# Kernel optimization log

Measured on AMD Instinct MI355X. Metric: run time of the kernel, lower is better.

Reference implementation:

```python
import jax, jax.numpy as jnp
import numpy as np

GATE_THRESH = 0.4
ALPHA_FN = lambda L: 1.0 - 1.0 / L  # length-adaptive alpha, called with actual L
EPS_NORM = 1e-12  # F.normalize eps
EPS_LN = 1e-5     # LayerNorm eps


def setup_inputs() -> dict:
    key = jax.random.key(0)
    B, L, H, V = 64, 2048, 128, 32000
    ks = jax.random.split(key, 8)
    s = lambda k, shape, fan: jax.random.normal(k, shape, jnp.float32) * (1.0 / np.sqrt(fan))
    return {
        "seq": jax.random.randint(ks[0], (B, L), 0, V, dtype=jnp.int64),
        "embed_w": jax.random.normal(ks[1], (V, H), jnp.float32) * 0.02,
        "ff_w1": s(ks[2], (2 * H, H), H), "ff_b1": jnp.zeros((2 * H,), jnp.float32),
        "ff_w2": s(ks[3], (H, 2 * H), 2 * H), "ff_b2": jnp.zeros((H,), jnp.float32),
        "ln_g": jnp.ones((H,), jnp.float32), "ln_b": jnp.zeros((H,), jnp.float32),
        "kp_w": s(ks[4], (H, H), H),
        "rp_w": s(ks[5], (H, H), H), "rp_b": jnp.zeros((H,), jnp.float32),
        "out_w": s(ks[6], (V, H), H), "out_b": jnpp if False else jnp.zeros((V,), jnp.float32),
    }


def reference(seq, embed_w, ff_w1, ff_b1, ff_w2, ff_b2, ln_g, ln_b, kp_w, rp_w, rp_b, out_w, out_b):
    h = embed_w[seq]                                            # [B,L,H]
    ff = jnp.maximum(h @ ff_w1.T + ff_b1, 0.0) @ ff_w2.T + ff_b2
    x = h + ff
    mu = x.mean(-1, keepdims=True)
    var = x.var(-1, keepdims=True)                              # biased, as LayerNorm
    h = (x - mu) / jnp.sqrt(var + EPS_LN) * ln_g + ln_b
    B, L, H = h.shape
    alpha = ALPHA_FN(L)
    k_all = jnp.einsum('blh,oh->blo', h, kp_w)                  # kp has no bias

    def step(M, k):                                             # M:[B,H,H], k:[B,H]
        kn = k / jnp.maximum(jnp.linalg.norm(k, axis=-1, keepdims=True), EPS_NORM)
        vp = jnp.einsum('bij,bj->bi', M, kn)
        d = k - vp
        delta = d[:, :, None] * kn[:, None, :]                  # outer product [B,H,H]
        fire = (jnp.linalg.norm(d, axis=-1) >= GATE_THRESH * jnp.linalg.norm(k, axis=-1)).astype(k.dtype)
        return M + (1.0 - alpha) * fire[:, None, None] * delta, None

    M0 = jnp.zeros((B, H, H), h.dtype)
    M, _ = jax.lax.scan(step, M0, jnp.swapaxes(k_all[:, :-1, :], 0, 1))  # scan over L-1 steps
    q = k_all[:, -1, :]
    read = jnp.einsum('bij,bj->bi', M, q)
    return (read @ rp_w.T + rp_b) @ out_w.T + out_b             # [B,V]
```

## Files before the change

### kernel.cpp

```cpp
#include <hip/hip_runtime.h>
#include <hip/hip_bf16.h>
#include <stdint.h>

#define Bn 64
#define Ln 2048
#define Hn 128
#define Vn 32000
#define THn 256
#define LAMBDA_ (1.0f/2048.0f)
#define CC 32
#define NCH (Ln/CC)
#define KP  132
#define KTS 36
#define VS  132
#define VPW (CC*VS)
#define ADS 131
#define ADW (CC*ADS+4)
#define GS  36
#define GXS 33
#define MSR 36
#define MSW 576
#define HS  132

typedef short bf16x8 __attribute__((ext_vector_type(8)));
typedef float f32x4  __attribute__((ext_vector_type(4)));

__device__ __forceinline__ float rdlane(float v, int s) {
  return __int_as_float(__builtin_amdgcn_readlane(__float_as_int(v), s));
}

template <int CTRL>
__device__ __forceinline__ float dpp_add(float x) {
  int t = __builtin_amdgcn_update_dpp(0, __float_as_int(x), CTRL, 0xf, 0xf, false);
  return x + __int_as_float(t);
}
__device__ __forceinline__ float wave_sum64(float x) {
  x = dpp_add<0x111>(x);
  x = dpp_add<0x112>(x);
  x = dpp_add<0x114>(x);
  x = dpp_add<0x118>(x);
  x = dpp_add<0x142>(x);
  x = dpp_add<0x143>(x);
  return rdlane(x, 63);
}

__device__ __forceinline__ uint32_t packhl(float x) {
  uint32_t bx = __float_as_uint(x);
  float hf = __uint_as_float(bx & 0xFFFF0000u);
  uint32_t bl = __float_as_uint(x - hf);
  return (bx >> 16) | (bl & 0xFFFF0000u);
}
__device__ __forceinline__ float unpackhl(uint32_t u) {
  return __uint_as_float(u << 16) + __uint_as_float(u & 0xFFFF0000u);
}

struct FragHL { bf16x8 h; bf16x8 l; };
__device__ __forceinline__ FragHL mkfrag(const uint32_t* u) {
  union { uint32_t a[4]; bf16x8 v; } H, L;
  H.a[0] = __builtin_amdgcn_perm(u[1], u[0], 0x05040100u);
  H.a[1] = __builtin_amdgcn_perm(u[3], u[2], 0x05040100u);
  H.a[2] = __builtin_amdgcn_perm(u[5], u[4], 0x05040100u);
  H.a[3] = __builtin_amdgcn_perm(u[7], u[6], 0x05040100u);
  L.a[0] = __builtin_amdgcn_perm(u[1], u[0], 0x07060302u);
  L.a[1] = __builtin_amdgcn_perm(u[3], u[2], 0x07060302u);
  L.a[2] = __builtin_amdgcn_perm(u[5], u[4], 0x07060302u);
  L.a[3] = __builtin_amdgcn_perm(u[7], u[6], 0x07060302u);
  FragHL f; f.h = H.v; f.l = L.v; return f;
}

__device__ __forceinline__ void ld8(const uint32_t* p, uint32_t* u) {
  const uint4 a = *reinterpret_cast<const uint4*>(p);
  const uint4 b = *reinterpret_cast<const uint4*>(p + 4);
  u[0]=a.x; u[1]=a.y; u[2]=a.z; u[3]=a.w;
  u[4]=b.x; u[5]=b.y; u[6]=b.z; u[7]=b.w;
}

__device__ __forceinline__ bf16x8 asbf(uint4 u) {
  union { uint4 a; bf16x8 v; } c; c.a = u; return c.v;
}

__device__ __forceinline__ f32x4 mfma16(bf16x8 a, bf16x8 b, f32x4 c) {
  return __builtin_amdgcn_mfma_f32_16x16x32_bf16(a, b, c, 0, 0, 0);
}

__device__ __forceinline__ void gload_lds4(const uint32_t* g, uint32_t* l) {
  __builtin_amdgcn_global_load_lds(
      (const __attribute__((address_space(1))) void*)g,
      (__attribute__((address_space(3))) void*)l, 4, 0, 0);
}

__global__ __launch_bounds__(256) void p0_pack(
    const float* __restrict__ w1, const float* __restrict__ w2,
    const float* __restrict__ kp, uint32_t* __restrict__ wp)
{
  const int id = blockIdx.x*256 + threadIdx.x;
  const float* src; uint32_t *dh, *dl; int p;
  if (id < 16384)      { src = w1; p = id;         dh = wp;         dl = wp+16384; }
  else if (id < 32768) { src = w2; p = id-16384;   dh = wp+32768;   dl = wp+49152; }
  else                 { src = kp; p = id-32768;   dh = wp+65536;   dl = wp+73728; }
  const float x0 = src[2*p], x1 = src[2*p+1];
  const uint32_t b0 = __float_as_uint(x0), b1 = __float_as_uint(x1);
  const float l0f = x0 - __uint_as_float(b0 & 0xFFFF0000u);
  const float l1f = x1 - __uint_as_float(b1 & 0xFFFF0000u);
  dh[p] = (b0 >> 16) | ((b1 >> 16) << 16);
  dl[p] = (__float_as_uint(l0f) >> 16) | ((__float_as_uint(l1f) >> 16) << 16);
}

__global__ __launch_bounds__(256, 2) void p1_fused(
    const int* __restrict__ seq,
    const float* __restrict__ embed_w,
    const uint32_t* __restrict__ wp,
    const float* __restrict__ ff_b1, const float* __restrict__ ff_b2,
    const float* __restrict__ ln_g, const float* __restrict__ ln_b,
    uint32_t* __restrict__ knp_all, float* __restrict__ norm_all)
{
  __shared__ __align__(16) uint32_t h_p[64*HS];
  __shared__ __align__(16) uint32_t u_p[64*HS];
  __shared__ float part1[256], part2[256];
  __shared__ float mul[64], rsl[64];
  __shared__ int sid[64];

  const int tid  = threadIdx.x;
  const int lane = tid & 63;
  const int w    = __builtin_amdgcn_readfirstlane(tid >> 6);
  const int q4   = lane >> 4;
  const int m16  = lane & 15;
  const int tile0 = blockIdx.x * 64;

  const uint32_t* w1h = wp;
  const uint32_t* w1l = wp + 16384;
  const uint32_t* w2h = wp + 32768;
  const uint32_t* w2l = wp + 49152;
  const uint32_t* kph = wp + 65536;
  const uint32_t* kpl = wp + 73728;

  if (tid < 64) sid[tid] = seq[tile0 + tid];
  __syncthreads();

  {
    const int t = tid >> 2, part = tid & 3;
    const float4* erow =
        reinterpret_cast<const float4*>(embed_w + (size_t)sid[t]*Hn) + part*8;
    #pragma unroll
    for (int c = 0; c < 8; ++c) {
      float4 v = erow[c];
      int j = part*32 + c*4;
      h_p[t*HS+j+0] = packhl(v.x); h_p[t*HS+j+1] = packhl(v.y);
      h_p[t*HS+j+2] = packhl(v.z); h_p[t*HS+j+3] = packhl(v.w);
    }
  }
  __syncthreads();

  f32x4 acc2[4][2];
  #pragma unroll
  for (int tt=0;tt<4;++tt)
    #pragma unroll
    for (int ct=0;ct<2;++ct) acc2[tt][ct] = (f32x4){0.f,0.f,0.f,0.f};

  #pragma unroll 1
  for (int ho=0; ho<2; ++ho) {
    #pragma unroll 1
    for (int tt=0; tt<4; ++tt) {
      FragHL fa[4];
      #pragma unroll
      for (int kk=0;kk<4;++kk) {
        uint32_t ua[8];
        ld8(&h_p[(16*tt+m16)*HS + 32*kk + 8*q4], ua);
        fa[kk] = mkfrag(ua);
      }
      #pragma unroll
      for (int ct=0; ct<2; ++ct) {
        const int ob = 128*ho + 32*w + 16*ct;
        f32x4 a = (f32x4){0.f,0.f,0.f,0.f};
        #pragma unroll
        for (int kk=0;kk<4;++kk) {
          const size_t wi = (size_t)(ob+m16)*64 + 16*kk + 4*q4;
          bf16x8 bh = asbf(*reinterpret_cast<const uint4*>(&w1h[wi]));
          bf16x8 bl = asbf(*reinterpret_cast<const uint4*>(&w1l[wi]));
          a = mfma16(fa[kk].h, bh, a);
          a = mfma16(fa[kk].h, bl, a);
          a = mfma16(fa[kk].l, bh, a);
        }
        const float bb = ff_b1[ob + m16];
        #pragma unroll
        for (int reg=0;reg<4;++reg) {
          float uv = fmaxf(a[reg] + bb, 0.f);
          u_p[(16*tt+4*q4+reg)*HS + 32*w + 16*ct + m16] = packhl(uv);
        }
      }
    }
    __syncthreads();
    #pragma unroll 1
    for (int tt=0; tt<4; ++tt) {
      FragHL fu[4];
      #pragma unroll
      for (int kk=0;kk<4;++kk) {
        uint32_t ua[8];
        ld8(&u_p[(16*tt+m16)*HS + 32*kk + 8*q4], ua);
        fu[kk] = mkfrag(ua);
      }
      #pragma unroll
      for (int ct=0; ct<2; ++ct) {
        const int ib = 32*w + 16*ct;
        f32x4 a = acc2[tt][ct];
        #pragma unroll
        for (int kk=0;kk<4;++kk) {
          const size_t wi = (size_t)(ib+m16)*128 + 64*ho + 16*kk + 4*q4;
          bf16x8 bh = asbf(*reinterpret_cast<const uint4*>(&w2h[wi]));
          bf16x8 bl = asbf(*reinterpret_cast<const uint4*>(&w2l[wi]));
          a = mfma16(fu[kk].h, bh, a);
          a = mfma16(fu[kk].h, bl, a);
          a = mfma16(fu[kk].l, bh, a);
        }
        acc2[tt][ct] = a;
      }
    }
    __syncthreads();
  }

  float xx[4][2][4];
  #pragma unroll
  for (int tt=0;tt<4;++tt)
    #pragma unroll
    for (int ct=0;ct<2;++ct) {
      const int col = 32*w + 16*ct + m16;
      const float b2 = ff_b2[col];
      #pragma unroll
      for (int reg=0;reg<4;++reg) {
        const float hval = unpackhl(h_p[(16*tt+4*q4+reg)*HS + col]);
        xx[tt][ct][reg] = acc2[tt][ct][reg] + b2 + hval;
      }
    }
  #pragma unroll
  for (int tt=0;tt<4;++tt)
    #pragma unroll
    for (int reg=0;reg<4;++reg) {
      float s1 = xx[tt][0][reg] + xx[tt][1][reg];
      float s2 = xx[tt][0][reg]*xx[tt][0][reg] + xx[tt][1][reg]*xx[tt][1][reg];
      s1 += __shfl_xor(s1,1); s1 += __shfl_xor(s1,2);
      s1 += __shfl_xor(s1,4); s1 += __shfl_xor(s1,8);
      s2 += __shfl_xor(s2,1); s2 += __shfl_xor(s2,2);
      s2 += __shfl_xor(s2,4); s2 += __shfl_xor(s2,8);
      if (m16==0) {
        part1[w*64 + 16*tt+4*q4+reg] = s1;
        part2[w*64 + 16*tt+4*q4+reg] = s2;
      }
    }
  __syncthreads();
  if (tid < 64) {
    const float mu = (part1[tid]+part1[64+tid]+part1[128+tid]+part1[192+tid])*(1.0f/128.0f);
    const float ms = (part2[tid]+part2[64+tid]+part2[128+tid]+part2[192+tid])*(1.0f/128.0f);
    mul[tid] = mu;
    rsl[tid] = rsqrtf(ms - mu*mu + 1e-5f);
  }
  __syncthreads();

  #pragma unroll
  for (int tt=0;tt<4;++tt)
    #pragma unroll
    for (int ct=0;ct<2;++ct) {
      const int col = 32*w + 16*ct + m16;
      const float g = ln_g[col], bb = ln_b[col];
      #pragma unroll
      for (int reg=0;reg<4;++reg) {
        const int tok = 16*tt+4*q4+reg;
        const float hn = (xx[tt][ct][reg] - mul[tok])*rsl[tok]*g + bb;
        h_p[tok*HS + col] = packhl(hn);
      }
    }
  __syncthreads();

  f32x4 ak[4][2];
  #pragma unroll 1
  for (int tt=0;tt<4;++tt) {
    FragHL fh[4];
    #pragma unroll
    for (int kk=0;kk<4;++kk) {
      uint32_t ua[8];
      ld8(&h_p[(16*tt+m16)*HS + 32*kk + 8*q4], ua);
      fh[kk] = mkfrag(ua);
    }
    #pragma unroll
    for (int ct=0;ct<2;++ct) {
      const int ob = 32*w + 16*ct;
      f32x4 a = (f32x4){0.f,0.f,0.f,0.f};
      #pragma unroll
      for (int kk=0;kk<4;++kk) {
        const size_t wi = (size_t)(ob+m16)*64 + 16*kk + 4*q4;
        bf16x8 bh = asbf(*reinterpret_cast<const uint4*>(&kph[wi]));
        bf16x8 bl = asbf(*reinterpret_cast<const uint4*>(&kpl[wi]));
        a = mfma16(fh[kk].h, bh, a);
        a = mfma16(fh[kk].h, bl, a);
        a = mfma16(fh[kk].l, bh, a);
      }
      ak[tt][ct] = a;
    }
  }
  #pragma unroll
  for (int tt=0;tt<4;++tt)
    #pragma unroll
    for (int reg=0;reg<4;++reg) {
      float s = ak[tt][0][reg]*ak[tt][0][reg] + ak[tt][1][reg]*ak[tt][1][reg];
      s += __shfl_xor(s,1); s += __shfl_xor(s,2);
      s += __shfl_xor(s,4); s += __shfl_xor(s,8);
      if (m16==0) part1[w*64 + 16*tt+4*q4+reg] = s;
    }
  __syncthreads();
  if (tid < 64) {
    const float nn = part1[tid]+part1[64+tid]+part1[128+tid]+part1[192+tid];
    const float nrm = sqrtf(nn);
    norm_all[tile0 + tid] = nrm;
    mul[tid] = 1.0f / fmaxf(nrm, 1e-12f);
  }
  __syncthreads();
  #pragma unroll
  for (int tt=0;tt<4;++tt)
    #pragma unroll
    for (int ct=0;ct<2;++ct) {
      const int col = 32*w + 16*ct + m16;
      #pragma unroll
      for (int reg=0;reg<4;++reg) {
        const int tok = 16*tt+4*q4+reg;
        knp_all[(size_t)(tile0+tok)*Hn + col] = packhl(ak[tt][ct][reg]*mul[tok]);
      }
    }
}

__global__ __launch_bounds__(768, 3) void p2_scan(
    const uint32_t* __restrict__ knp_all, const float* __restrict__ norm_all,
    float* __restrict__ read_ws)
{
  const int tid  = threadIdx.x;
  const int lane = tid & 63;
  const int wv   = __builtin_amdgcn_readfirstlane(tid >> 6);
  const int q    = lane >> 4;
  const int m    = lane & 15;
  const int b    = blockIdx.x;

  __shared__ __align__(16) uint32_t kn_p[2*CC*KP];
  __shared__ __align__(16) uint32_t knT [128*KTS];
  __shared__ __align__(16) float    vp0L[2*VPW];
  __shared__ __align__(16) float    adL [2*ADW];
  __shared__ __align__(16) float    Gt  [2*CC*GS];
  __shared__ __align__(16) float    GxT [CC*GXS];
  __shared__ __align__(16) uint32_t msc [8*MSW];
  __shared__ float nrm_l[4*CC];

  const uint32_t* knb = knp_all + (size_t)b*Ln*Hn;
  const float*    nb  = norm_all + (size_t)b*Ln;

  const int swm  = ((m>>3)&3)<<3;
  const int swm2 = (((16+m)>>3)&3)<<3;

  {
    if (tid < 256) {
      const int t = tid>>3, g = tid&7;
      const int sw = ((t>>3)&3)<<3;
      const uint4* src = reinterpret_cast<const uint4*>(knb + t*Hn + g*16);
      uint32_t* dstb = &kn_p[t*KP];
      *reinterpret_cast<uint4*>(&dstb[(16*g+0) ^ sw])  = src[0];
      *reinterpret_cast<uint4*>(&dstb[(16*g+4) ^ sw])  = src[1];
      *reinterpret_cast<uint4*>(&dstb[(16*g+8) ^ sw])  = src[2];
      *reinterpret_cast<uint4*>(&dstb[(16*g+12) ^ sw]) = src[3];
    } else if (tid < 512) {
      const int idx = tid-256, t = idx>>3, g = idx&7;
      const int sw = ((t>>3)&3)<<3;
      const uint4* src = reinterpret_cast<const uint4*>(knb + CC*Hn + t*Hn + g*16);
      uint32_t* dstb = &kn_p[CC*KP + t*KP];
      *reinterpret_cast<uint4*>(&dstb[(16*g+0) ^ sw])  = src[0];
      *reinterpret_cast<uint4*>(&dstb[(16*g+4) ^ sw])  = src[1];
      *reinterpret_cast<uint4*>(&dstb[(16*g+8) ^ sw])  = src[2];
      *reinterpret_cast<uint4*>(&dstb[(16*g+12) ^ sw]) = src[3];
    } else if (tid < 512+2*CC) {
      nrm_l[tid-512] = nb[tid-512];
    }
  }
  __syncthreads();

  {
    if (wv >= 9) {
      const int gi = wv - 9;
      if (gi < 3) {
        const int ti = (gi==2) ? 1 : 0;
        const int si = (gi==0) ? 0 : 1;
        const int ra = 16*ti+m, rb = 16*si+m;
        const int swa = ((ra>>3)&3)<<3, swb = ((rb>>3)&3)<<3;
        f32x4 g4 = (f32x4){0.f,0.f,0.f,0.f};
        #pragma unroll
        for (int kk=0; kk<4; ++kk) {
          uint32_t ua[8], ub[8];
          ld8(&kn_p[ra*KP + ((32*kk + 8*q) ^ swa)], ua);
          ld8(&kn_p[rb*KP + ((32*kk + 8*q) ^ swb)], ub);
          FragHL fa = mkfrag(ua), fb = mkfrag(ub);
          g4 = mfma16(fa.h, fb.h, g4);
          g4 = mfma16(fa.h, fb.l, g4);
          g4 = mfma16(fa.l, fb.h, g4);
        }
        #pragma unroll
        for (int reg=0; reg<4; ++reg)
          Gt[(16*ti + 4*q + reg)*GS + 16*si + m] = g4[reg];
        if (gi==1) {
          #pragma unroll
          for (int reg=0; reg<4; ++reg)
            Gt[(16*si + m)*GS + 16*ti + 4*q + reg] = g4[reg];
        }
      }
    }
    if (wv >= 1 && wv <= 8) {
      const int h0 = 16*(wv-1);
      const float nr0 = nrm_l[m], nr1 = nrm_l[16+m];
      const uint4 r0 = *reinterpret_cast<const uint4*>(&kn_p[m*KP + ((h0 + 4*q) ^ swm)]);
      const uint4 r1 = *reinterpret_cast<const uint4*>(&kn_p[(16+m)*KP + ((h0 + 4*q) ^ swm2)]);
      const uint32_t* pr0 = &r0.x; const uint32_t* pr1 = &r1.x;
      #pragma unroll
      for (int reg=0; reg<4; ++reg) {
        const int h = h0 + 4*q + reg;
        vp0L[m*VS + h]      = nr0*unpackhl(pr0[reg]);
        vp0L[(16+m)*VS + h] = nr1*unpackhl(pr1[reg]);
      }
    }
  }
  __syncthreads();

  if (wv == 0) {
    #pragma unroll 1
    for (int ch=0; ch<NCH; ++ch) {
      const int cur = ch&1;
      const int sel = ch & 1;
      const uint32_t* knc = &kn_p[cur*CC*KP];

      float ad0[CC], ad1[CC];
      float* adW = &adL[sel*ADW];
      const float* vpR = &vp0L[sel*VPW];
      const float* GtS = &Gt[sel*CC*GS];
      const int lid = lane & 31;
      const float nrmv = nrm_l[(ch&3)*CC + lid];
      float grt = GtS[0*GS + lid];
      float grn = GtS[1*GS + lid];
      __builtin_amdgcn_s_setprio(1);
      #pragma unroll
      for (int t=0;t<CC;++t) {
        float grn2 = 0.f;
        if (t+2 < CC) grn2 = GtS[(t+2)*GS + lid];
        float a0c0 = vpR[t*VS + lane];
        float a1c0 = vpR[t*VS + 64 + lane];
        float a0c1=0.f, a0c2=0.f, a0c3=0.f;
        float a1c1=0.f, a1c2=0.f, a1c3=0.f;
        #pragma unroll
        for (int s=0; s<t; ++s) {
          const float g = rdlane(grt, s);
          switch (s & 3) {
            case 0: a0c0 -= g*ad0[s]; a1c0 -= g*ad1[s]; break;
            case 1: a0c1 -= g*ad0[s]; a1c1 -= g*ad1[s]; break;
            case 2: a0c2 -= g*ad0[s]; a1c2 -= g*ad1[s]; break;
            default:a0c3 -= g*ad0[s]; a1c3 -= g*ad1[s]; break;
          }
        }
        const float acc0 = (a0c0+a0c1)+(a0c2+a0c3);
        const float acc1 = (a1c0+a1c1)+(a1c2+a1c3);
        const float sqt = wave_sum64(acc0*acc0 + acc1*acc1);
        const float nrm = rdlane(nrmv, t);
        if (ch==NCH-1 && t==CC-1) {
          const int swt = ((t>>3)&3)<<3;
          const float kn0 = unpackhl(knc[t*KP + (lane ^ swt)]);
          const float kn1 = unpackhl(knc[t*KP + ((64+lane) ^ swt)]);
          read_ws[b*Hn + lane]      = nrm*(nrm*kn0 - acc0);
          read_ws[b*Hn + 64 + lane] = nrm*(nrm*kn1 - acc1);
        } else {
          const float at = (sqt >= 0.16f*nrm*nrm) ? LAMBDA_ : 0.f;
          ad0[t] = at*acc0; ad1[t] = at*acc1;
          adW[t*ADS + lane]      = ad0[t];
          adW[t*ADS + 64 + lane] = ad1[t];
        }
        grt = grn; grn = grn2;
      }
      __builtin_amdgcn_s_setprio(0);

      __syncthreads();
      if (ch==NCH-1) break;
      __syncthreads();
    }
  } else if (wv <= 8) {
    f32x4 Macc[8];
    #pragma unroll
    for (int ct=0; ct<8; ++ct) Macc[ct] = (f32x4){0.f,0.f,0.f,0.f};
    const int h0 = 16*(wv-1);

    #pragma unroll 1
    for (int ch=0; ch<NCH; ++ch) {
      const int cur = ch&1, nx1 = (ch+1)&1;
      const int sel = ch & 1;
      const uint32_t* knN = &kn_p[nx1*CC*KP];
      const bool havn  = (ch+1 < NCH);
      const bool havn2 = (ch+2 < NCH);

      float pfn = 0.f;
      if (havn2 && tid >= 288 && tid < 320) pfn = nb[(ch+2)*CC + (tid-288)];

      if (havn) {
        if (ch >= 1) {
          const float* adR = &adL[(1-sel)*ADW];
          uint32_t ap[8];
          #pragma unroll
          for (int j=0;j<8;++j)
            ap[j] = packhl(adR[(8*q+j)*ADS + h0 + m]);
          FragHL fa = mkfrag(ap);
          #pragma unroll
          for (int ct=0; ct<8; ++ct) {
            const int hcol = 16*ct + m;
            const int swz = ((hcol>>3)&3)<<3;
            uint32_t bu[8];
            ld8(&knT[hcol*KTS + (8*q ^ swz)], bu);
            FragHL fb = mkfrag(bu);
            Macc[ct] = mfma16(fa.h, fb.h, Macc[ct]);
            Macc[ct] = mfma16(fa.h, fb.l, Macc[ct]);
            Macc[ct] = mfma16(fa.l, fb.h, Macc[ct]);
          }
        }
        {
          f32x4 v0 = (f32x4){0.f,0.f,0.f,0.f};
          f32x4 v1 = (f32x4){0.f,0.f,0.f,0.f};
          uint32_t* mybase = &msc[(wv-1)*MSW];
          #pragma unroll
          for (int kk=0; kk<4; ++kk) {
            #pragma unroll
            for (int c2=0; c2<2; ++c2) {
              const int ct = 2*kk + c2;
              #pragma unroll
              for (int reg=0; reg<4; ++reg)
                mybase[(4*q+reg)*MSR + 16*c2 + m] = packhl(Macc[ct][reg]);
            }
            uint32_t ua[8], ub[8];
            ld8(&mybase[m*MSR + 8*q], ua);
            FragHL fa = mkfrag(ua);
            ld8(&knN[m*KP + ((32*kk + 8*q) ^ swm)], ub);
            FragHL fb = mkfrag(ub);
            v0 = mfma16(fa.h, fb.h, v0);
            v0 = mfma16(fa.h, fb.l, v0);
            v0 = mfma16(fa.l, fb.h, v0);
            ld8(&knN[(16+m)*KP + ((32*kk + 8*q) ^ swm2)], ub);
            fb = mkfrag(ub);
            v1 = mfma16(fa.h, fb.h, v1);
            v1 = mfma16(fa.h, fb.l, v1);
            v1 = mfma16(fa.l, fb.h, v1);
          }
          float* vpW = &vp0L[(1-sel)*VPW];
          const float nr0 = nrm_l[((ch+1)&3)*CC + m];
          const float nr1 = nrm_l[((ch+1)&3)*CC + 16 + m];
          const uint4 r0 = *reinterpret_cast<const uint4*>(&knN[m*KP + ((h0 + 4*q) ^ swm)]);
          const uint4 r1 = *reinterpret_cast<const uint4*>(&knN[(16+m)*KP + ((h0 + 4*q) ^ swm2)]);
          const uint32_t* pr0 = &r0.x; const uint32_t* pr1 = &r1.x;
          #pragma unroll
          for (int reg=0; reg<4; ++reg) {
            const int h = h0 + 4*q + reg;
            vpW[m*VS + h]      = nr0*unpackhl(pr0[reg]) - v0[reg];
            vpW[(16+m)*VS + h] = nr1*unpackhl(pr1[reg]) - v1[reg];
          }
        }
      }

      __syncthreads();
      if (ch==NCH-1) break;

      {
        uint2 tv[4];
        #pragma unroll
        for (int r=0; r<4; ++r) {
          const int t = (wv-1)*4 + r;
          tv[r] = *reinterpret_cast<const uint2*>(
              &knb[(size_t)ch*CC*Hn + t*Hn + 2*lane]);
        }

        f32x4 c0 = (f32x4){0.f,0.f,0.f,0.f};
        f32x4 c1 = (f32x4){0.f,0.f,0.f,0.f};
        {
          const float* adR = &adL[sel*ADW];
          uint32_t* mybase = &msc[(wv-1)*MSW];
          #pragma unroll
          for (int c2=0; c2<2; ++c2)
            #pragma unroll
            for (int reg=0; reg<4; ++reg)
              mybase[(4*q+reg)*MSR + 16*c2 + m] =
                  packhl(adR[(16*c2+m)*ADS + h0 + 4*q + reg]);
          uint32_t ua[8], gb[8];
          ld8(&mybase[m*MSR + 8*q], ua);
          FragHL fa = mkfrag(ua);
          #pragma unroll
          for (int jj=0;jj<8;++jj) gb[jj] = packhl(GxT[m*GXS + 8*q + jj]);
          FragHL fb = mkfrag(gb);
          c0 = mfma16(fa.h, fb.h, c0);
          c0 = mfma16(fa.h, fb.l, c0);
          c0 = mfma16(fa.l, fb.h, c0);
          #pragma unroll
          for (int jj=0;jj<8;++jj) gb[jj] = packhl(GxT[(16+m)*GXS + 8*q + jj]);
          fb = mkfrag(gb);
          c1 = mfma16(fa.h, fb.h, c1);
          c1 = mfma16(fa.h, fb.l, c1);
          c1 = mfma16(fa.l, fb.h, c1);
        }
        {
          float* vpW = &vp0L[(1-sel)*VPW];
          #pragma unroll
          for (int reg=0; reg<4; ++reg) {
            const int h = h0 + 4*q + reg;
            vpW[m*VS + h]      -= c0[reg];
            vpW[(16+m)*VS + h] -= c1[reg];
          }
        }
        {
          const int h2 = 2*lane;
          const int swz = ((h2>>3)&3)<<3;
          #pragma unroll
          for (int r=0; r<4; ++r) {
            const int t = (wv-1)*4 + r;
            knT[h2*KTS     + (t ^ swz)] = tv[r].x;
            knT[(h2+1)*KTS + (t ^ swz)] = tv[r].y;
          }
        }
        if (havn2) {
          const uint32_t* gsrc = knb + (size_t)(ch+2)*CC*Hn;
          uint32_t* ldst = &kn_p[cur*CC*KP];
          #pragma unroll
          for (int r=0; r<4; ++r) {
            const int t = (wv-1)*4 + r;
            const int sw = ((t>>3)&3)<<3;
            #pragma unroll
            for (int half=0; half<2; ++half) {
              gload_lds4(gsrc + t*Hn + ((half*64 + lane) ^ sw),
                         &ldst[t*KP + half*64]);
            }
          }
          if (tid >= 288 && tid < 320) nrm_l[((ch+2)&3)*CC + (tid-288)] = pfn;
        }
      }
      __syncthreads();
    }
  } else if (wv <= 10) {
    const int tj = wv - 9;
    #pragma unroll 1
    for (int ch=0; ch<NCH; ++ch) {
      const int cur = ch&1, nx1 = (ch+1)&1;
      const uint32_t* knc = &kn_p[cur*CC*KP];
      const uint32_t* knN = &kn_p[nx1*CC*KP];
      const bool havn = (ch+1 < NCH);

      if (havn) {
        #pragma unroll
        for (int ts=0; ts<2; ++ts) {
          const int ra = 16*tj+m, rb = 16*ts+m;
          const int swa = ((ra>>3)&3)<<3, swb = ((rb>>3)&3)<<3;
          f32x4 g4 = (f32x4){0.f,0.f,0.f,0.f};
          #pragma unroll
          for (int kk=0; kk<4; ++kk) {
            uint32_t ua[8], ub[8];
            ld8(&knN[ra*KP + ((32*kk + 8*q) ^ swa)], ua);
            ld8(&knc[rb*KP + ((32*kk + 8*q) ^ swb)], ub);
            FragHL fa = mkfrag(ua), fb = mkfrag(ub);
            g4 = mfma16(fa.h, fb.h, g4);
            g4 = mfma16(fa.h, fb.l, g4);
            g4 = mfma16(fa.l, fb.h, g4);
          }
          #pragma unroll
          for (int reg=0; reg<4; ++reg)
            GxT[(16*tj + 4*q + reg)*GXS + 16*ts + m] = g4[reg];
        }
      }
      __syncthreads();
      if (ch==NCH-1) break;
      __syncthreads();
    }
  } else {
    #pragma unroll 1
    for (int ch=0; ch<NCH; ++ch) {
      const int nx1 = (ch+1)&1;
      const int sel = ch & 1;
      const uint32_t* knN = &kn_p[nx1*CC*KP];
      const bool havn = (ch+1 < NCH);

      if (havn) {
        #pragma unroll
        for (int gi=0; gi<3; ++gi) {
          const int ti = (gi==2) ? 1 : 0;
          const int si = (gi==0) ? 0 : 1;
          const int ra = 16*ti+m, rb = 16*si+m;
          const int swa = ((ra>>3)&3)<<3, swb = ((rb>>3)&3)<<3;
          f32x4 g4 = (f32x4){0.f,0.f,0.f,0.f};
          #pragma unroll
          for (int kk=0; kk<4; ++kk) {
            uint32_t ua[8], ub[8];
            ld8(&knN[ra*KP + ((32*kk + 8*q) ^ swa)], ua);
            ld8(&knN[rb*KP + ((32*kk + 8*q) ^ swb)], ub);
            FragHL fa = mkfrag(ua), fb = mkfrag(ub);
            g4 = mfma16(fa.h, fb.h, g4);
            g4 = mfma16(fa.h, fb.l, g4);
            g4 = mfma16(fa.l, fb.h, g4);
          }
          float* GtW = &Gt[(1-sel)*CC*GS];
          #pragma unroll
          for (int reg=0; reg<4; ++reg)
            GtW[(16*ti + 4*q + reg)*GS + 16*si + m] = g4[reg];
          if (gi==1) {
            #pragma unroll
            for (int reg=0; reg<4; ++reg)
              GtW[(16*si + m)*GS + 16*ti + 4*q + reg] = g4[reg];
          }
        }
      }
      __syncthreads();
      if (ch==NCH-1) break;
      __syncthreads();
    }
  }
}

__global__ __launch_bounds__(128) void p3a(
    const float* __restrict__ read_ws, const float* __restrict__ rp_w,
    const float* __restrict__ rp_b, float* __restrict__ o1_ws)
{
  __shared__ float rd[128];
  const int b = blockIdx.x, t = threadIdx.x;
  rd[t] = read_ws[b*Hn + t];
  __syncthreads();
  float acc = rp_b[t];
  const float* wr = rp_w + t*Hn;
  #pragma unroll 4
  for (int i = 0; i < Hn; ++i) acc += rd[i]*wr[i];
  o1_ws[b*Hn + t] = acc;
}

__global__ __launch_bounds__(256) void p3b(
    const float* __restrict__ o1_ws, const float* __restrict__ out_w,
    const float* __restrict__ out_b, float* __restrict__ out)
{
  __shared__ __align__(16) float o1[8192];
  const int tid = threadIdx.x;
  #pragma unroll
  for (int c = 0; c < 32; ++c) o1[c*256+tid] = o1_ws[c*256+tid];
  __syncthreads();
  const int v = blockIdx.x*256 + tid;
  float acc[64];
  const float ob = out_b[v];
  #pragma unroll
  for (int bb = 0; bb < 64; ++bb) acc[bb] = ob;
  const float4* wrow = reinterpret_cast<const float4*>(out_w + (size_t)v*Hn);
  #pragma unroll 1
  for (int r4 = 0; r4 < 32; ++r4) {
    const float4 wv = wrow[r4];
    #pragma unroll
    for (int bb = 0; bb < 64; ++bb) {
      const float4 ov = *reinterpret_cast<const float4*>(&o1[bb*Hn + r4*4]);
      acc[bb] += wv.x*ov.x + wv.y*ov.y + wv.z*ov.z + wv.w*ov.w;
    }
  }
  #pragma unroll
  for (int bb = 0; bb < 64; ++bb) out[(size_t)bb*Vn + v] = acc[bb];
}

extern "C" void kernel_launch(void* const* d_in, const int* in_sizes, int n_in,
                              void* d_out, int out_size, void* d_ws, size_t ws_size,
                              hipStream_t stream)
{
  const int*   seq     = (const int*)  d_in[0];
  const float* embed_w = (const float*)d_in[1];
  const float* ff_w1   = (const float*)d_in[2];
  const float* ff_b1   = (const float*)d_in[3];
  const float* ff_w2   = (const float*)d_in[4];
  const float* ff_b2   = (const float*)d_in[5];
  const float* ln_g    = (const float*)d_in[6];
  const float* ln_b    = (const float*)d_in[7];
  const float* kp_w    = (const float*)d_in[8];
  const float* rp_w    = (const float*)d_in[9];
  const float* rp_b    = (const float*)d_in[10];
  const float* out_w   = (const float*)d_in[11];
  const float* out_b   = (const float*)d_in[12];

  float* ws          = (float*)d_ws;
  uint32_t* knp_all  = (uint32_t*)ws;
  float* norm_all    = ws + (size_t)Bn*Ln*Hn;
  float* read_ws     = norm_all + (size_t)Bn*Ln;
  float* o1_ws       = read_ws + Bn*Hn;
  uint32_t* wp       = (uint32_t*)(o1_ws + Bn*Hn);

  p0_pack<<<dim3(160), dim3(256), 0, stream>>>(ff_w1, ff_w2, kp_w, wp);
  p1_fused<<<dim3(2048), dim3(256), 0, stream>>>(
      seq, embed_w, wp, ff_b1, ff_b2, ln_g, ln_b, knp_all, norm_all);
  p2_scan<<<dim3(64), dim3(768), 0, stream>>>(knp_all, norm_all, read_ws);
  p3a<<<dim3(64), dim3(128), 0, stream>>>(read_ws, rp_w, rp_b, o1_ws);
  p3b<<<dim3(125), dim3(256), 0, stream>>>(o1_ws, out_w, out_b, (float*)d_out);
}
```

Before: 695.2 us.

## Store scan deltas pre-packed transposed in LDS and reuse MFMA fragment across stages

The serial wave now writes its gated delta vectors straight into a transposed, XOR-swizzled packed hi/lo buffer instead of a padded float buffer. The MFMA waves then build their A fragment with one vector LDS load and keep it in registers for the next chunk's M update, instead of repacking through a scratch buffer twice. GxT gets a swizzled layout so it can be read with float4 loads. The aim is to cut LDS traffic, bank conflicts and packing work on the per-chunk critical path, at the cost of carrying an extra fragment in registers across the loop and depending on correct swizzle indexing and synchronisation between the stages.

```diff
diff --git a/kernel.cpp b/kernel.cpp
--- a/kernel.cpp
+++ b/kernel.cpp
@@ -12,12 +12,11 @@
 #define NCH (Ln/CC)
 #define KP  132
 #define KTS 36
+#define ADT 36
 #define VS  132
 #define VPW (CC*VS)
-#define ADS 131
-#define ADW (CC*ADS+4)
 #define GS  36
-#define GXS 33
+#define GXS 36
 #define MSR 36
 #define MSW 576
 #define HS  132
@@ -339,8 +338,8 @@
 
   __shared__ __align__(16) uint32_t kn_p[2*CC*KP];
   __shared__ __align__(16) uint32_t knT [128*KTS];
+  __shared__ __align__(16) uint32_t adT [128*ADT];
   __shared__ __align__(16) float    vp0L[2*VPW];
-  __shared__ __align__(16) float    adL [2*ADW];
   __shared__ __align__(16) float    Gt  [2*CC*GS];
   __shared__ __align__(16) float    GxT [CC*GXS];
   __shared__ __align__(16) uint32_t msc [8*MSW];
@@ -423,6 +422,7 @@
   __syncthreads();
 
   if (wv == 0) {
+    const int swl = ((lane>>3)&3)<<3;
     #pragma unroll 1
     for (int ch=0; ch<NCH; ++ch) {
       const int cur = ch&1;
@@ -430,7 +430,6 @@
       const uint32_t* knc = &kn_p[cur*CC*KP];
 
       float ad0[CC], ad1[CC];
-      float* adW = &adL[sel*ADW];
       const float* vpR = &vp0L[sel*VPW];
       const float* GtS = &Gt[sel*CC*GS];
       const int lid = lane & 31;
@@ -469,8 +468,8 @@
         } else {
           const float at = (sqt >= 0.16f*nrm*nrm) ? LAMBDA_ : 0.f;
           ad0[t] = at*acc0; ad1[t] = at*acc1;
-          adW[t*ADS + lane]      = ad0[t];
-          adW[t*ADS + 64 + lane] = ad1[t];
+          adT[lane*ADT + (t ^ swl)]      = packhl(ad0[t]);
+          adT[(64+lane)*ADT + (t ^ swl)] = packhl(ad1[t]);
         }
         grt = grn; grn = grn2;
       }
@@ -485,6 +484,8 @@
     #pragma unroll
     for (int ct=0; ct<8; ++ct) Macc[ct] = (f32x4){0.f,0.f,0.f,0.f};
     const int h0 = 16*(wv-1);
+    FragHL faAD;
+    { uint32_t z[8] = {0,0,0,0,0,0,0,0}; faAD = mkfrag(z); }
 
     #pragma unroll 1
     for (int ch=0; ch<NCH; ++ch) {
@@ -499,12 +500,6 @@
 
       if (havn) {
         if (ch >= 1) {
-          const float* adR = &adL[(1-sel)*ADW];
-          uint32_t ap[8];
-          #pragma unroll
-          for (int j=0;j<8;++j)
-            ap[j] = packhl(adR[(8*q+j)*ADS + h0 + m]);
-          FragHL fa = mkfrag(ap);
           #pragma unroll
           for (int ct=0; ct<8; ++ct) {
             const int hcol = 16*ct + m;
@@ -512,9 +507,9 @@
             uint32_t bu[8];
             ld8(&knT[hcol*KTS + (8*q ^ swz)], bu);
             FragHL fb = mkfrag(bu);
-            Macc[ct] = mfma16(fa.h, fb.h, Macc[ct]);
-            Macc[ct] = mfma16(fa.h, fb.l, Macc[ct]);
-            Macc[ct] = mfma16(fa.l, fb.h, Macc[ct]);
+            Macc[ct] = mfma16(faAD.h, fb.h, Macc[ct]);
+            Macc[ct] = mfma16(faAD.h, fb.l, Macc[ct]);
+            Macc[ct] = mfma16(faAD.l, fb.h, Macc[ct]);
           }
         }
         {
@@ -571,32 +566,46 @@
               &knb[(size_t)ch*CC*Hn + t*Hn + 2*lane]);
         }
 
+        {
+          const int rowA = h0 + m;
+          const int swa = ((rowA>>3)&3)<<3;
+          uint32_t ua[8];
+          ld8(&adT[rowA*ADT + (8*q ^ swa)], ua);
+          faAD = mkfrag(ua);
+        }
         f32x4 c0 = (f32x4){0.f,0.f,0.f,0.f};
         f32x4 c1 = (f32x4){0.f,0.f,0.f,0.f};
         {
-          const float* adR = &adL[sel*ADW];
-          uint32_t* mybase = &msc[(wv-1)*MSW];
-          #pragma unroll
-          for (int c2=0; c2<2; ++c2)
-            #pragma unroll
-            for (int reg=0; reg<4; ++reg)
-              mybase[(4*q+reg)*MSR + 16*c2 + m] =
-                  packhl(adR[(16*c2+m)*ADS + h0 + 4*q + reg]);
-          uint32_t ua[8], gb[8];
-          ld8(&mybase[m*MSR + 8*q], ua);
-          FragHL fa = mkfrag(ua);
-          #pragma unroll
-          for (int jj=0;jj<8;++jj) gb[jj] = packhl(GxT[m*GXS + 8*q + jj]);
-          FragHL fb = mkfrag(gb);
-          c0 = mfma16(fa.h, fb.h, c0);
-          c0 = mfma16(fa.h, fb.l, c0);
-          c0 = mfma16(fa.l, fb.h, c0);
-          #pragma unroll
-          for (int jj=0;jj<8;++jj) gb[jj] = packhl(GxT[(16+m)*GXS + 8*q + jj]);
-          fb = mkfrag(gb);
-          c1 = mfma16(fa.h, fb.h, c1);
-          c1 = mfma16(fa.h, fb.l, c1);
-          c1 = mfma16(fa.l, fb.h, c1);
+          const int swg = (m&3)<<3;
+          uint32_t gbu[8];
+          {
+            const float4 ga = *reinterpret_cast<const float4*>(
+                &GxT[m*GXS + (8*q ^ swg)]);
+            const float4 gc = *reinterpret_cast<const float4*>(
+                &GxT[m*GXS + (8*q ^ swg) + 4]);
+            gbu[0]=packhl(ga.x); gbu[1]=packhl(ga.y);
+            gbu[2]=packhl(ga.z); gbu[3]=packhl(ga.w);
+            gbu[4]=packhl(gc.x); gbu[5]=packhl(gc.y);
+            gbu[6]=packhl(gc.z); gbu[7]=packhl(gc.w);
+          }
+          FragHL fb = mkfrag(gbu);
+          c0 = mfma16(faAD.h, fb.h, c0);
+          c0 = mfma16(faAD.h, fb.l, c0);
+          c0 = mfma16(faAD.l, fb.h, c0);
+          {
+            const float4 ga = *reinterpret_cast<const float4*>(
+                &GxT[(16+m)*GXS + (8*q ^ swg)]);
+            const float4 gc = *reinterpret_cast<const float4*>(
+                &GxT[(16+m)*GXS + (8*q ^ swg) + 4]);
+            gbu[0]=packhl(ga.x); gbu[1]=packhl(ga.y);
+            gbu[2]=packhl(ga.z); gbu[3]=packhl(ga.w);
+            gbu[4]=packhl(gc.x); gbu[5]=packhl(gc.y);
+            gbu[6]=packhl(gc.z); gbu[7]=packhl(gc.w);
+          }
+          fb = mkfrag(gbu);
+          c1 = mfma16(faAD.h, fb.h, c1);
+          c1 = mfma16(faAD.h, fb.l, c1);
+          c1 = mfma16(faAD.l, fb.h, c1);
         }
         {
           float* vpW = &vp0L[(1-sel)*VPW];
@@ -662,7 +671,7 @@
           }
           #pragma unroll
           for (int reg=0; reg<4; ++reg)
-            GxT[(16*tj + 4*q + reg)*GXS + 16*ts + m] = g4[reg];
+            GxT[(16*tj + 4*q + reg)*GXS + ((16*ts + m) ^ (reg<<3))] = g4[reg];
         }
       }
       __syncthreads();
```

Result: slower. 719.8 us (+3.5%).
